# Kernel optimization log

Hardware: AMD Instinct MI355X
Metric: run time of the kernel (lower is better)

The kernel has to match this reference:

```python
import jax, jax.numpy as jnp
import numpy as np

BOUND = 3.0
MIN_BIN_W = 1e-3   # min_bin_width
MIN_BIN_H = 1e-3   # min_bin_height
MIN_DERIV = 1e-3   # min_derivative
MIN_LAMBDA = 0.025
EPS = 1e-6


def _knots(frac, min_size, left, right):
    # frac: [D, K] normalized (softmax) bin fractions -> (bin sizes [D,K], knot positions [D,K+1])
    K = frac.shape[-1]
    sizes = min_size + (1.0 - min_size * K) * frac
    cum = jnp.cumsum(sizes, axis=-1)
    cum = jnp.concatenate([jnp.zeros_like(cum[..., :1]), cum], axis=-1)
    cum = (right - left) * cum + left
    cum = cum.at[..., 0].set(left)
    cum = cum.at[..., -1].set(right)
    sizes = cum[..., 1:] - cum[..., :-1]
    return sizes, cum


def _spline_fwd(x, uw, uh, ud, ul, bound=BOUND):
    # x: [B, D]; uw/uh/ul: [D, K]; ud: [D, K-1]
    B, D = x.shape
    K = uw.shape[-1]
    w = jax.nn.softmax(uw, axis=-1)
    h = jax.nn.softmax(uh, axis=-1)
    d = MIN_DERIV + jax.nn.softplus(ud)
    lam = MIN_LAMBDA + (1.0 - 2.0 * MIN_LAMBDA) * jax.nn.sigmoid(ul)

    left, right = -bound, bound
    widths, cumwidths = _knots(w, MIN_BIN_W, left, right)
    heights, cumheights = _knots(h, MIN_BIN_H, left, right)
    ones = jnp.ones_like(d[..., :1])
    derivs = jnp.concatenate([ones, d, ones], axis=-1)  # [D, K+1]; identity slope at the tails

    inside = (x >= left) & (x <= right)
    xc = jnp.clip(x, left, right)  # keep spline branch NaN-free for outside points

    # bucketize: index of bin containing each input, per dimension  -> [B, D]
    bin_idx = jnp.sum(xc[..., None] >= (cumwidths + EPS)[None], axis=-1) - 1
    bin_idx = jnp.clip(bin_idx, 0, K - 1)

    def sel(t):
        # gather per-(sample, dim) bin parameter: t [D, K or K+1] -> [B, D]
        tb = jnp.broadcast_to(t[None], (B,) + t.shape)
        return jnp.take_along_axis(tb, bin_idx[..., None], axis=-1)[..., 0]

    iw, icw = sel(widths), sel(cumwidths)
    ih, ich = sel(heights), sel(cumheights)
    idelta = sel(heights / widths)
    d0, d1 = sel(derivs), sel(derivs[..., 1:])
    il = sel(lam)

    # monotonic *linear* rational spline (Dolatabadi et al.), forward direction
    wa = 1.0
    wb = jnp.sqrt(d0 / d1) * wa
    wc = (il * wa * d0 + (1.0 - il) * wb * d1) / idelta
    ya = ich
    yb = ih + ich
    yc = ((1.0 - il) * wa * ya + il * wb * yb) / ((1.0 - il) * wa + il * wb)

    theta = (xc - icw) / iw
    lo = theta <= il
    num = jnp.where(lo,
                    wa * ya * (il - theta) + wc * yc * theta,
                    wc * yc * (1.0 - theta) + wb * yb * (theta - il))
    den = jnp.where(lo,
                    wa * (il - theta) + wc * theta,
                    wc * (1.0 - theta) + wb * (theta - il))
    dnum = jnp.where(lo,
                     wa * wc * il * (yc - ya),
                     wb * wc * (1.0 - il) * (yb - yc)) / iw

    u = jnp.where(inside, num / den, x)                      # identity outside the box
    logabsdet = jnp.where(inside, jnp.log(dnum) - 2.0 * jnp.log(jnp.abs(den)), 0.0)
    return u, jnp.sum(logabsdet, axis=1)


def setup_inputs() -> dict:
    B, D, K = 32768, 256, 32
    key = jax.random.key(0)
    k1, k2, k3, k4, k5 = jax.random.split(key, 5)
    return {
        "x": jax.random.normal(k1, (B, D), jnp.float32),
        "uw": jax.random.normal(k2, (D, K), jnp.float32),
        "uh": jax.random.normal(k3, (D, K), jnp.float32),
        "ud": jax.random.normal(k4, (D, K - 1), jnp.float32),
        "ul": jax.random.uniform(k5, (D, K), jnp.float32),
    }


def reference(x, uw, uh, ud, ul):
    # f: data x -> latent u, plus log|det J| summed over feature dim
    return _spline_fwd(x, uw, uh, ud, ul)
```

## Files before the change

kernel.cpp:

```cpp
#include <hip/hip_runtime.h>
#include <hip/hip_fp16.h>
#include <math.h>
#include <stdint.h>

#define D_DIM 256
#define K_BINS 32
#define NCELL 1024
#define ENT4_STRIDE 132
#define LIC_STRIDE 34
#define LUT_BSTRIDE 1028
#define SLICE 16

static constexpr float BOUND = 3.0f;
static constexpr float MIN_BIN_W = 1e-3f;
static constexpr float MIN_DERIV = 1e-3f;
static constexpr float MIN_LAMBDA = 0.025f;
static constexpr float EPS_ = 1e-6f;
static constexpr float CELL_W = 6.0f / NCELL;
static constexpr float CELL_S = NCELL / 6.0f;
static constexpr float LN2_ = 0.69314718055994531f;

__device__ __forceinline__ float softplusf_(float x) {
  return fmaxf(x, 0.0f) + log1pf(expf(-fabsf(x)));
}

__device__ __forceinline__ float pack2h_as_f32(float a, float b) {
  __half2 h = __halves2half2(__float2half_rn(a), __float2half_rn(b));
  union { __half2 h; uint32_t u; } c;
  c.h = h;
  return __uint_as_float(c.u);
}

__device__ __forceinline__ float2 unpack2h_from_f32(float v) {
  union { uint32_t u; __half2 h; } c;
  c.u = __float_as_uint(v);
  return make_float2(__low2float(c.h), __high2float(c.h));
}

__device__ __forceinline__ float dpp_quadsum4(float v) {
  int t;
  t = __builtin_amdgcn_update_dpp(0, __float_as_int(v), 0xB1, 0xF, 0xF, false);
  v += __int_as_float(t);
  t = __builtin_amdgcn_update_dpp(0, __float_as_int(v), 0x4E, 0xF, 0xF, false);
  v += __int_as_float(t);
  return v;
}

__device__ __forceinline__ void eval1(
    float xv, int dml,
    const float* lentA, const float* lentB,
    const float* lic, const uint8_t* lutb,
    float& uu_out, float& lad2_out) {
  float xc = fminf(fmaxf(xv, -BOUND), BOUND);
  bool inside = fabsf(xv) <= BOUND;

  float cf = fmaf(xc, CELL_S, (float)(NCELL / 2));
  int c = (int)cf;
  c = min(c, NCELL - 1);
  int ilut = (int)lutb[dml * LUT_BSTRIDE + c];

  float c1 = lic[dml * LIC_STRIDE + ilut + 1];
  int idx = ilut + (xc >= c1 ? 1 : 0);

  int eb = dml * ENT4_STRIDE + idx * 4;
  float4 A = *reinterpret_cast<const float4*>(&lentA[eb]);
  float4 Bv = *reinterpret_cast<const float4*>(&lentB[eb]);

  float icw = A.x, inv_iw = A.y, il = A.z, wcv = A.w;
  float wbv = Bv.x, yc = Bv.y;
  float2 dd = unpack2h_from_f32(Bv.z);
  float2 LL = unpack2h_from_f32(Bv.w);

  float theta = (xc - icw) * inv_iw;
  bool lo = theta <= il;
  float t1 = il - theta;
  float t3 = 1.0f - theta;

  float den = lo ? fmaf(wcv, theta, t1)
                 : fmaf(wcv, t3, -(wbv * t1));
  float sfac = lo ? dd.x : (wbv * dd.y);
  float Ls = lo ? LL.x : LL.y;

  float r = __builtin_amdgcn_rcpf(den);
  float uu = fmaf(-t1 * sfac, r, yc);
  float lad2 = fmaf(-2.0f, __builtin_amdgcn_logf(den), Ls);

  uu_out = inside ? uu : xv;
  lad2_out = inside ? lad2 : 0.0f;
}

__global__ __launch_bounds__(512) void spline_fused(
    const float* __restrict__ x,
    const float* __restrict__ uw,
    const float* __restrict__ uh,
    const float* __restrict__ ud,
    const float* __restrict__ ul,
    float* __restrict__ uout,
    float* __restrict__ part,
    int B) {
  __shared__ __align__(16) float lentA[SLICE * ENT4_STRIDE];
  __shared__ __align__(16) float lentB[SLICE * ENT4_STRIDE];
  __shared__ float lic[SLICE * LIC_STRIDE];
  __shared__ uint8_t lutb[SLICE * LUT_BSTRIDE];

  int tid = threadIdx.x;
  int slice = blockIdx.x & 15;
  int group = blockIdx.x >> 4;
  int d0 = slice * SLICE;

  {
    int k = tid & 31;
    int dim = tid >> 5;
    int d = d0 + dim;

    float uwv = uw[d * K_BINS + k];
    float uhv = uh[d * K_BINS + k];
    float ulv = ul[d * K_BINS + k];
    float udv = (k < K_BINS - 1) ? ud[d * (K_BINS - 1) + k] : 0.0f;

    float wm = uwv, hm = uhv;
    for (int o = 16; o; o >>= 1) {
      wm = fmaxf(wm, __shfl_xor(wm, o, 32));
      hm = fmaxf(hm, __shfl_xor(hm, o, 32));
    }
    float ew = expf(uwv - wm), eh = expf(uhv - hm);
    float ws = ew, hs = eh;
    for (int o = 16; o; o >>= 1) {
      ws += __shfl_xor(ws, o, 32);
      hs += __shfl_xor(hs, o, 32);
    }
    const float kfac = 1.0f - MIN_BIN_W * (float)K_BINS;
    float sw = MIN_BIN_W + kfac * (ew / ws);
    float sh = MIN_BIN_W + kfac * (eh / hs);

    float cws = sw, chs = sh;
    for (int o = 1; o < 32; o <<= 1) {
      float tw = __shfl_up(cws, o, 32);
      float th = __shfl_up(chs, o, 32);
      if (k >= o) { cws += tw; chs += th; }
    }
    const float scale = 2.0f * BOUND;
    float raw_w = scale * cws - BOUND;
    float raw_h = scale * chs - BOUND;
    float upw = __shfl_up(raw_w, 1, 32);
    float uph = __shfl_up(raw_h, 1, 32);
    float cw_lo = (k == 0) ? -BOUND : upw;
    float ch_lo = (k == 0) ? -BOUND : uph;
    float cw_hi = (k == K_BINS - 1) ? BOUND : raw_w;
    float ch_hi = (k == K_BINS - 1) ? BOUND : raw_h;

    float iw = cw_hi - cw_lo;
    float ih = ch_hi - ch_lo;

    float dk = MIN_DERIV + softplusf_(udv);
    float dprev = __shfl_up(dk, 1, 32);
    float d1 = (k == K_BINS - 1) ? 1.0f : dk;
    float dd0 = (k == 0) ? 1.0f : dprev;

    float sg = 1.0f / (1.0f + expf(-ulv));
    float lam = MIN_LAMBDA + (1.0f - 2.0f * MIN_LAMBDA) * sg;

    float wb = sqrtf(dd0 / d1);
    float delta = ih / iw;
    float wc = (lam * dd0 + (1.0f - lam) * wb * d1) / delta;
    float denom = (1.0f - lam) + lam * wb;
    float dyc = lam * wb * ih / denom;
    float dyb = ih - dyc;
    float ya = ch_lo;
    float inv_iw = 1.0f / iw;
    float yc = ya + dyc;

    float* eA = &lentA[dim * ENT4_STRIDE + k * 4];
    eA[0] = cw_lo;
    eA[1] = inv_iw;
    eA[2] = lam;
    eA[3] = wc;
    float* eB = &lentB[dim * ENT4_STRIDE + k * 4];
    eB[0] = wb;
    eB[1] = yc;
    eB[2] = pack2h_as_f32(dyc, dyb);
    eB[3] = pack2h_as_f32(log2f(wc * lam * dyc * inv_iw),
                          log2f(wc * wb * (1.0f - lam) * dyb * inv_iw));

    float t = cw_lo + EPS_;
    lic[dim * LIC_STRIDE + k] = t;
    if (k == 0) lic[dim * LIC_STRIDE + 32] = 1e30f;

    int c0 = 0;
    if (k > 0) {
      float q = (t + BOUND + 1e-5f) * CELL_S;
      c0 = (int)ceilf(q);
      if (c0 < 0) c0 = 0;
      if (c0 > NCELL) c0 = NCELL;
      while (c0 < NCELL && (fmaf((float)c0, CELL_W, -BOUND) - 1e-5f) < t) ++c0;
      while (c0 > 0 && (fmaf((float)(c0 - 1), CELL_W, -BOUND) - 1e-5f) >= t) --c0;
    }
    int c1 = __shfl_down(c0, 1, 32);
    if (k == K_BINS - 1) c1 = NCELL;
    for (int c = c0; c < c1; ++c) lutb[dim * LUT_BSTRIDE + c] = (uint8_t)k;
  }
  __syncthreads();

  int lane = tid & 63;
  int wid = tid >> 6;
  int dq = lane & 3;
  int rsub = lane >> 2;
  int dml0 = dq * 4;

  int row0 = group * 512 + wid * 16 + rsub;
  size_t base = (size_t)row0 * D_DIM + d0 + dml0;
  float* parts = part + (size_t)slice * B;
  const size_t ISTEP = (size_t)128 * D_DIM;

  float4 xv = *reinterpret_cast<const float4*>(x + base);

#pragma unroll
  for (int it = 0; it < 4; ++it) {
    float4 xn;
    if (it < 3) xn = *reinterpret_cast<const float4*>(x + base + (size_t)(it + 1) * ISTEP);

    float u0, u1, u2, u3, l0, l1, l2, l3;
    eval1(xv.x, dml0 + 0, lentA, lentB, lic, lutb, u0, l0);
    eval1(xv.y, dml0 + 1, lentA, lentB, lic, lutb, u1, l1);
    eval1(xv.z, dml0 + 2, lentA, lentB, lic, lutb, u2, l2);
    eval1(xv.w, dml0 + 3, lentA, lentB, lic, lutb, u3, l3);

    float4 uv = make_float4(u0, u1, u2, u3);
    *reinterpret_cast<float4*>(uout + base + (size_t)it * ISTEP) = uv;

    float ls = (l0 + l1) + (l2 + l3);
    ls = dpp_quadsum4(ls);
    if (dq == 0) parts[row0 + it * 128] = ls;

    xv = xn;
  }
}

__global__ void spline_reduce(const float* __restrict__ part,
                              float* __restrict__ ldout, int B) {
  int row = blockIdx.x * 256 + threadIdx.x;
  if (row >= B) return;
  float s = 0.0f;
#pragma unroll
  for (int sl = 0; sl < D_DIM / SLICE; ++sl) s += part[(size_t)sl * B + row];
  ldout[row] = s * LN2_;
}

extern "C" void kernel_launch(void* const* d_in, const int* in_sizes, int n_in,
                              void* d_out, int out_size, void* d_ws, size_t ws_size,
                              hipStream_t stream) {
  const float* x  = (const float*)d_in[0];
  const float* uw = (const float*)d_in[1];
  const float* uh = (const float*)d_in[2];
  const float* ud = (const float*)d_in[3];
  const float* ul = (const float*)d_in[4];

  int B = in_sizes[0] / D_DIM;

  float* out = (float*)d_out;
  float* uout = out;
  float* ldout = out + (size_t)B * D_DIM;

  float* partw = (float*)d_ws;

  spline_fused<<<1024, 512, 0, stream>>>(x, uw, uh, ud, ul, uout, partw, B);
  spline_reduce<<<(B + 255) / 256, 256, 0, stream>>>(partw, ldout, B);
}
```

Before: 28.32 us.

## Precompute per-slice spline tables once in a separate kernel and copy into LDS

Moves the softmax, cumsum, knot, coefficient and bin-LUT construction out of the main kernel into a small precompute kernel that writes one table image per 16-dim slice to workspace. Each of the 1024 main blocks then just copies its slice image into LDS with float4 loads, instead of recomputing the same tables 64 times. This removes redundant transcendental and shuffle work and the serial byte-wise LUT fill from the main kernel's prologue. In exchange it adds an extra kernel launch and a dependent global round trip.

```diff
diff --git a/kernel.cpp b/kernel.cpp
--- a/kernel.cpp
+++ b/kernel.cpp
@@ -10,6 +10,12 @@
 #define LIC_STRIDE 34
 #define LUT_BSTRIDE 1028
 #define SLICE 16
+
+#define IMG_A 0
+#define IMG_B 2112
+#define IMG_LIC 4224
+#define IMG_LUT 4768
+#define IMG_DW 8880
 
 static constexpr float BOUND = 3.0f;
 static constexpr float MIN_BIN_W = 1e-3f;
@@ -46,6 +52,124 @@
   return v;
 }
 
+__global__ void spline_precompute(const float* __restrict__ uw,
+                                  const float* __restrict__ uh,
+                                  const float* __restrict__ ud,
+                                  const float* __restrict__ ul,
+                                  float* __restrict__ img) {
+  __shared__ uint8_t lut8[8 * LUT_BSTRIDE];
+
+  int tid = threadIdx.x;
+  int k = tid & 31;
+  int dsub = tid >> 5;
+  int d = blockIdx.x * 8 + dsub;
+  int s = d >> 4;
+  int ds = d & 15;
+  float* im = img + (size_t)s * IMG_DW;
+
+  float uwv = uw[d * K_BINS + k];
+  float uhv = uh[d * K_BINS + k];
+  float ulv = ul[d * K_BINS + k];
+  float udv = (k < K_BINS - 1) ? ud[d * (K_BINS - 1) + k] : 0.0f;
+
+  float wm = uwv, hm = uhv;
+  for (int o = 16; o; o >>= 1) {
+    wm = fmaxf(wm, __shfl_xor(wm, o, 32));
+    hm = fmaxf(hm, __shfl_xor(hm, o, 32));
+  }
+  float ew = expf(uwv - wm), eh = expf(uhv - hm);
+  float ws = ew, hs = eh;
+  for (int o = 16; o; o >>= 1) {
+    ws += __shfl_xor(ws, o, 32);
+    hs += __shfl_xor(hs, o, 32);
+  }
+  const float kfac = 1.0f - MIN_BIN_W * (float)K_BINS;
+  float sw = MIN_BIN_W + kfac * (ew / ws);
+  float sh = MIN_BIN_W + kfac * (eh / hs);
+
+  float cws = sw, chs = sh;
+  for (int o = 1; o < 32; o <<= 1) {
+    float tw = __shfl_up(cws, o, 32);
+    float th = __shfl_up(chs, o, 32);
+    if (k >= o) { cws += tw; chs += th; }
+  }
+  const float scale = 2.0f * BOUND;
+  float raw_w = scale * cws - BOUND;
+  float raw_h = scale * chs - BOUND;
+  float upw = __shfl_up(raw_w, 1, 32);
+  float uph = __shfl_up(raw_h, 1, 32);
+  float cw_lo = (k == 0) ? -BOUND : upw;
+  float ch_lo = (k == 0) ? -BOUND : uph;
+  float cw_hi = (k == K_BINS - 1) ? BOUND : raw_w;
+  float ch_hi = (k == K_BINS - 1) ? BOUND : raw_h;
+
+  float iw = cw_hi - cw_lo;
+  float ih = ch_hi - ch_lo;
+
+  float dk = MIN_DERIV + softplusf_(udv);
+  float dprev = __shfl_up(dk, 1, 32);
+  float d1 = (k == K_BINS - 1) ? 1.0f : dk;
+  float dd0 = (k == 0) ? 1.0f : dprev;
+
+  float sg = 1.0f / (1.0f + expf(-ulv));
+  float lam = MIN_LAMBDA + (1.0f - 2.0f * MIN_LAMBDA) * sg;
+
+  float wb = sqrtf(dd0 / d1);
+  float delta = ih / iw;
+  float wc = (lam * dd0 + (1.0f - lam) * wb * d1) / delta;
+  float denom = (1.0f - lam) + lam * wb;
+  float dyc = lam * wb * ih / denom;
+  float dyb = ih - dyc;
+  float ya = ch_lo;
+  float inv_iw = 1.0f / iw;
+  float yc = ya + dyc;
+
+  float* eA = im + IMG_A + ds * ENT4_STRIDE + k * 4;
+  eA[0] = cw_lo;
+  eA[1] = inv_iw;
+  eA[2] = lam;
+  eA[3] = wc;
+  float* eB = im + IMG_B + ds * ENT4_STRIDE + k * 4;
+  eB[0] = wb;
+  eB[1] = yc;
+  eB[2] = pack2h_as_f32(dyc, dyb);
+  eB[3] = pack2h_as_f32(log2f(wc * lam * dyc * inv_iw),
+                        log2f(wc * wb * (1.0f - lam) * dyb * inv_iw));
+
+  float t = cw_lo + EPS_;
+  im[IMG_LIC + ds * LIC_STRIDE + k] = t;
+  if (k == 0) im[IMG_LIC + ds * LIC_STRIDE + 32] = 1e30f;
+
+  int c0 = 0;
+  if (k > 0) {
+    float q = (t + BOUND + 1e-5f) * CELL_S;
+    c0 = (int)ceilf(q);
+    if (c0 < 0) c0 = 0;
+    if (c0 > NCELL) c0 = NCELL;
+    while (c0 < NCELL && (fmaf((float)c0, CELL_W, -BOUND) - 1e-5f) < t) ++c0;
+    while (c0 > 0 && (fmaf((float)(c0 - 1), CELL_W, -BOUND) - 1e-5f) >= t) --c0;
+  }
+  int c1 = __shfl_down(c0, 1, 32);
+  if (k == K_BINS - 1) c1 = NCELL;
+
+  {
+    uint8_t* lr = &lut8[dsub * LUT_BSTRIDE];
+    int c = c0;
+    while (c < c1 && (c & 3)) { lr[c] = (uint8_t)k; ++c; }
+    uint32_t kw = (uint32_t)k * 0x01010101u;
+    for (; c + 4 <= c1; c += 4) *reinterpret_cast<uint32_t*>(&lr[c]) = kw;
+    while (c < c1) { lr[c] = (uint8_t)k; ++c; }
+  }
+  __syncthreads();
+
+  {
+    const uint32_t* l32 = reinterpret_cast<const uint32_t*>(lut8);
+    int ds0 = (blockIdx.x & 1) * 8;
+    uint32_t* dst = reinterpret_cast<uint32_t*>(im + IMG_LUT) + ds0 * (LUT_BSTRIDE / 4);
+    for (int i = tid; i < 8 * (LUT_BSTRIDE / 4); i += 256) dst[i] = l32[i];
+  }
+}
+
 __device__ __forceinline__ void eval1(
     float xv, int dml,
     const float* lentA, const float* lentB,
@@ -89,19 +213,13 @@
   lad2_out = inside ? lad2 : 0.0f;
 }
 
-__global__ __launch_bounds__(512) void spline_fused(
+__global__ __launch_bounds__(512) void spline_main(
     const float* __restrict__ x,
-    const float* __restrict__ uw,
-    const float* __restrict__ uh,
-    const float* __restrict__ ud,
-    const float* __restrict__ ul,
+    const float* __restrict__ img,
     float* __restrict__ uout,
     float* __restrict__ part,
     int B) {
-  __shared__ __align__(16) float lentA[SLICE * ENT4_STRIDE];
-  __shared__ __align__(16) float lentB[SLICE * ENT4_STRIDE];
-  __shared__ float lic[SLICE * LIC_STRIDE];
-  __shared__ uint8_t lutb[SLICE * LUT_BSTRIDE];
+  __shared__ __align__(16) float ldsflat[IMG_DW];
 
   int tid = threadIdx.x;
   int slice = blockIdx.x & 15;
@@ -109,97 +227,16 @@
   int d0 = slice * SLICE;
 
   {
-    int k = tid & 31;
-    int dim = tid >> 5;
-    int d = d0 + dim;
-
-    float uwv = uw[d * K_BINS + k];
-    float uhv = uh[d * K_BINS + k];
-    float ulv = ul[d * K_BINS + k];
-    float udv = (k < K_BINS - 1) ? ud[d * (K_BINS - 1) + k] : 0.0f;
-
-    float wm = uwv, hm = uhv;
-    for (int o = 16; o; o >>= 1) {
-      wm = fmaxf(wm, __shfl_xor(wm, o, 32));
-      hm = fmaxf(hm, __shfl_xor(hm, o, 32));
-    }
-    float ew = expf(uwv - wm), eh = expf(uhv - hm);
-    float ws = ew, hs = eh;
-    for (int o = 16; o; o >>= 1) {
-      ws += __shfl_xor(ws, o, 32);
-      hs += __shfl_xor(hs, o, 32);
-    }
-    const float kfac = 1.0f - MIN_BIN_W * (float)K_BINS;
-    float sw = MIN_BIN_W + kfac * (ew / ws);
-    float sh = MIN_BIN_W + kfac * (eh / hs);
-
-    float cws = sw, chs = sh;
-    for (int o = 1; o < 32; o <<= 1) {
-      float tw = __shfl_up(cws, o, 32);
-      float th = __shfl_up(chs, o, 32);
-      if (k >= o) { cws += tw; chs += th; }
-    }
-    const float scale = 2.0f * BOUND;
-    float raw_w = scale * cws - BOUND;
-    float raw_h = scale * chs - BOUND;
-    float upw = __shfl_up(raw_w, 1, 32);
-    float uph = __shfl_up(raw_h, 1, 32);
-    float cw_lo = (k == 0) ? -BOUND : upw;
-    float ch_lo = (k == 0) ? -BOUND : uph;
-    float cw_hi = (k == K_BINS - 1) ? BOUND : raw_w;
-    float ch_hi = (k == K_BINS - 1) ? BOUND : raw_h;
-
-    float iw = cw_hi - cw_lo;
-    float ih = ch_hi - ch_lo;
-
-    float dk = MIN_DERIV + softplusf_(udv);
-    float dprev = __shfl_up(dk, 1, 32);
-    float d1 = (k == K_BINS - 1) ? 1.0f : dk;
-    float dd0 = (k == 0) ? 1.0f : dprev;
-
-    float sg = 1.0f / (1.0f + expf(-ulv));
-    float lam = MIN_LAMBDA + (1.0f - 2.0f * MIN_LAMBDA) * sg;
-
-    float wb = sqrtf(dd0 / d1);
-    float delta = ih / iw;
-    float wc = (lam * dd0 + (1.0f - lam) * wb * d1) / delta;
-    float denom = (1.0f - lam) + lam * wb;
-    float dyc = lam * wb * ih / denom;
-    float dyb = ih - dyc;
-    float ya = ch_lo;
-    float inv_iw = 1.0f / iw;
-    float yc = ya + dyc;
-
-    float* eA = &lentA[dim * ENT4_STRIDE + k * 4];
-    eA[0] = cw_lo;
-    eA[1] = inv_iw;
-    eA[2] = lam;
-    eA[3] = wc;
-    float* eB = &lentB[dim * ENT4_STRIDE + k * 4];
-    eB[0] = wb;
-    eB[1] = yc;
-    eB[2] = pack2h_as_f32(dyc, dyb);
-    eB[3] = pack2h_as_f32(log2f(wc * lam * dyc * inv_iw),
-                          log2f(wc * wb * (1.0f - lam) * dyb * inv_iw));
-
-    float t = cw_lo + EPS_;
-    lic[dim * LIC_STRIDE + k] = t;
-    if (k == 0) lic[dim * LIC_STRIDE + 32] = 1e30f;
-
-    int c0 = 0;
-    if (k > 0) {
-      float q = (t + BOUND + 1e-5f) * CELL_S;
-      c0 = (int)ceilf(q);
-      if (c0 < 0) c0 = 0;
-      if (c0 > NCELL) c0 = NCELL;
-      while (c0 < NCELL && (fmaf((float)c0, CELL_W, -BOUND) - 1e-5f) < t) ++c0;
-      while (c0 > 0 && (fmaf((float)(c0 - 1), CELL_W, -BOUND) - 1e-5f) >= t) --c0;
-    }
-    int c1 = __shfl_down(c0, 1, 32);
-    if (k == K_BINS - 1) c1 = NCELL;
-    for (int c = c0; c < c1; ++c) lutb[dim * LUT_BSTRIDE + c] = (uint8_t)k;
+    const float4* s4 = reinterpret_cast<const float4*>(img + (size_t)slice * IMG_DW);
+    float4* t4 = reinterpret_cast<float4*>(ldsflat);
+    for (int i = tid; i < IMG_DW / 4; i += 512) t4[i] = s4[i];
   }
   __syncthreads();
+
+  const float* lentA = ldsflat + IMG_A;
+  const float* lentB = ldsflat + IMG_B;
+  const float* lic   = ldsflat + IMG_LIC;
+  const uint8_t* lutb = reinterpret_cast<const uint8_t*>(ldsflat + IMG_LUT);
 
   int lane = tid & 63;
   int wid = tid >> 6;
@@ -261,8 +298,10 @@
   float* uout = out;
   float* ldout = out + (size_t)B * D_DIM;
 
-  float* partw = (float*)d_ws;
-
-  spline_fused<<<1024, 512, 0, stream>>>(x, uw, uh, ud, ul, uout, partw, B);
+  float* img = (float*)d_ws;
+  float* partw = (float*)((char*)d_ws + 16 * IMG_DW * 4);
+
+  spline_precompute<<<32, 256, 0, stream>>>(uw, uh, ud, ul, img);
+  spline_main<<<1024, 512, 0, stream>>>(x, img, uout, partw, B);
   spline_reduce<<<(B + 255) / 256, 256, 0, stream>>>(partw, ldout, B);
 }
```

Result: slower. 30.73 us (+8.5%).
